# Optimization experiments

Measured on AMD Instinct MI355X. Metric: run time of the kernel, lower is better.

Reference implementation:

```python
import jax, jax.numpy as jnp
import numpy as np

EPS = 1e-16


def setup_inputs() -> dict:
    key = jax.random.key(0)
    k1, k2 = jax.random.split(key)
    N, D = 512, 4096
    a = jax.random.normal(k1, (N, D), dtype=jnp.float32)
    p = jax.random.normal(k2, (N, D), dtype=jnp.float32)
    return {"a": a, "p": p}


def reference(a, p):
    N = a.shape[0]
    # Pairwise squared distances between anchors a and positives p:
    # ||a_i||^2 - 2 a_i . p_j + ||p_j||^2   (diag(a a^T) == row norms)
    dot = jnp.matmul(a, p.T)                       # [N, N]
    sq_a = jnp.sum(a * a, axis=-1)                 # [N]
    sq_p = jnp.sum(p * p, axis=-1)                 # [N]
    d2 = sq_a[:, None] - 2.0 * dot + sq_p[None, :]
    d2 = jnp.maximum(d2, 0.0)                      # distances[distances < 0] = 0
    zero_mask = (d2 == 0.0).astype(d2.dtype)
    dist = (1.0 - zero_mask) * jnp.sqrt(d2 + zero_mask * EPS)  # [N, N]

    # Triplet tensor: loss[a, p, n] = dist[a, p] - dist[a, n]
    triplet = dist[:, :, None] - dist[:, None, :]  # [N, N, N]

    # Validity mask: labels = arange(N) -> valid iff p == anchor and n != anchor
    labels = jnp.arange(N)
    label_eq = labels[:, None] == labels[None, :]  # [N, N]
    mask = label_eq[:, :, None] & (~label_eq[:, None, :])  # [N, N, N]

    triplet = mask.astype(triplet.dtype) * triplet
    triplet = jax.nn.relu(triplet)

    num_positive = jnp.sum(triplet > EPS).astype(triplet.dtype)
    loss = jnp.sum(triplet) / (num_positive + EPS)
    return loss
```

## Files before the change

### kernel.cpp

```cpp
#include <hip/hip_runtime.h>
#include <math.h>

#define PN 512
#define PD 4096

#define KSZ 8
#define KCHUNK (PD / KSZ)
#define BK 64
#define NSTAGE (KCHUNK / BK)

#define WS_AH_BYTES 8192
#define WS_PH_BYTES (8192 + 4194304)
#define WS_PART_FLOAT 2099200
#define WS_NEED_BF16 ((size_t)(8192 + 2 * 4194304 + (size_t)KSZ * PN * PN * 4))

typedef __attribute__((ext_vector_type(8))) short short8;
typedef __attribute__((ext_vector_type(4))) float floatx4;

static __device__ __forceinline__ unsigned short f2bf(float x) {
    unsigned int u = __float_as_uint(x);
    u += 0x7fffu + ((u >> 16) & 1u);
    return (unsigned short)(u >> 16);
}

static __device__ __forceinline__ void load16_lds(const void* gp, void* lp) {
    __builtin_amdgcn_global_load_lds(
        (const __attribute__((address_space(1))) unsigned int*)gp,
        (__attribute__((address_space(3))) unsigned int*)lp,
        16, 0, 0);
}

struct ushort4s { unsigned short x, y, z, w; };

__global__ __launch_bounds__(256) void taw_prep_kernel(
        const float* __restrict__ a, const float* __restrict__ p,
        float* __restrict__ ws) {
    const int i = blockIdx.x;
    const int t = threadIdx.x;
    if (i == 0 && t == 0) {
        ws[1536] = 0.0f;
        ((unsigned int*)ws)[1537] = 0u;
    }
    const float4* a4 = (const float4*)(a + (size_t)i * PD);
    const float4* p4 = (const float4*)(p + (size_t)i * PD);
    unsigned short* ah = (unsigned short*)((char*)ws + WS_AH_BYTES) + (size_t)i * PD;
    unsigned short* ph = (unsigned short*)((char*)ws + WS_PH_BYTES) + (size_t)i * PD;
    float sa = 0.f, sp = 0.f, dp = 0.f;
#pragma unroll
    for (int c = 0; c < 4; ++c) {
        const int e = c * 256 + t;
        float4 av = a4[e];
        float4 pv = p4[e];
        sa += av.x * av.x + av.y * av.y + av.z * av.z + av.w * av.w;
        sp += pv.x * pv.x + pv.y * pv.y + pv.z * pv.z + pv.w * pv.w;
        dp += av.x * pv.x + av.y * pv.y + av.z * pv.z + av.w * pv.w;
        ushort4s ab = {f2bf(av.x), f2bf(av.y), f2bf(av.z), f2bf(av.w)};
        ushort4s pb = {f2bf(pv.x), f2bf(pv.y), f2bf(pv.z), f2bf(pv.w)};
        *(ushort4s*)(ah + (size_t)e * 4) = ab;
        *(ushort4s*)(ph + (size_t)e * 4) = pb;
    }
#pragma unroll
    for (int off = 32; off > 0; off >>= 1) {
        sa += __shfl_down(sa, off, 64);
        sp += __shfl_down(sp, off, 64);
        dp += __shfl_down(dp, off, 64);
    }
    __shared__ float red[3][4];
    const int wave = t >> 6;
    if ((t & 63) == 0) { red[0][wave] = sa; red[1][wave] = sp; red[2][wave] = dp; }
    __syncthreads();
    if (t == 0) {
        sa = red[0][0] + red[0][1] + red[0][2] + red[0][3];
        sp = red[1][0] + red[1][1] + red[1][2] + red[1][3];
        dp = red[2][0] + red[2][1] + red[2][2] + red[2][3];
        float d2 = sa - 2.f * dp + sp;
        d2 = fmaxf(d2, 0.f);
        ws[i] = sa;
        ws[512 + i] = sp;
        ws[1024 + i] = (d2 == 0.f) ? 0.f : sqrtf(d2);
    }
}

__global__ __launch_bounds__(256) void taw_mfma_kernel(float* __restrict__ ws) {
    __shared__ short lds[2][8][64][8];
    const unsigned short* ah = (const unsigned short*)((const char*)ws + WS_AH_BYTES);
    const unsigned short* ph = (const unsigned short*)((const char*)ws + WS_PH_BYTES);
    const int t = threadIdx.x;
    const int lane = t & 63;
    const int w = t >> 6;
    const int wm = w >> 1, wn = w & 1;
    const int i0 = blockIdx.y * 64;
    const int j0 = blockIdx.x * 64;
    const int kz = blockIdx.z * KCHUNK;

    floatx4 acc[2][2] = {{{0.f, 0.f, 0.f, 0.f}, {0.f, 0.f, 0.f, 0.f}},
                         {{0.f, 0.f, 0.f, 0.f}, {0.f, 0.f, 0.f, 0.f}}};

    for (int st = 0; st < NSTAGE; ++st) {
        const int kb = kz + st * BK;
        __syncthreads();
#pragma unroll
        for (int q = 0; q < 2; ++q) {
            const int g = 2 * w + q;
            const int row = ((g & 3) << 4) + (lane & 15);
            const int kk = kb + ((((g >> 2) << 2) + (lane >> 4)) << 3);
            load16_lds(ah + (size_t)(i0 + row) * PD + kk, &lds[0][g][0][0]);
            load16_lds(ph + (size_t)(j0 + row) * PD + kk, &lds[1][g][0][0]);
        }
        __syncthreads();
#pragma unroll
        for (int s2 = 0; s2 < 2; ++s2) {
            short8 af0 = *(const short8*)&lds[0][s2 * 4 + wm * 2 + 0][lane][0];
            short8 af1 = *(const short8*)&lds[0][s2 * 4 + wm * 2 + 1][lane][0];
            short8 bf0 = *(const short8*)&lds[1][s2 * 4 + wn * 2 + 0][lane][0];
            short8 bf1 = *(const short8*)&lds[1][s2 * 4 + wn * 2 + 1][lane][0];
            acc[0][0] = __builtin_amdgcn_mfma_f32_16x16x32_bf16(af0, bf0, acc[0][0], 0, 0, 0);
            acc[0][1] = __builtin_amdgcn_mfma_f32_16x16x32_bf16(af0, bf1, acc[0][1], 0, 0, 0);
            acc[1][0] = __builtin_amdgcn_mfma_f32_16x16x32_bf16(af1, bf0, acc[1][0], 0, 0, 0);
            acc[1][1] = __builtin_amdgcn_mfma_f32_16x16x32_bf16(af1, bf1, acc[1][1], 0, 0, 0);
        }
    }

    float* part = ws + WS_PART_FLOAT + (size_t)blockIdx.z * (PN * PN);
    const int jj = j0 + wn * 32 + (lane & 15);
    const int ib = i0 + wm * 32 + ((lane >> 4) << 2);
#pragma unroll
    for (int rm = 0; rm < 2; ++rm)
#pragma unroll
        for (int rn = 0; rn < 2; ++rn)
#pragma unroll
            for (int r = 0; r < 4; ++r)
                part[(size_t)(ib + rm * 16 + r) * PN + jj + rn * 16] = acc[rm][rn][r];
}

__global__ __launch_bounds__(256) void taw_reduce_kernel(float* __restrict__ ws) {
    const int g = blockIdx.x * 256 + threadIdx.x;
    const float4* part4 = (const float4*)(ws + WS_PART_FLOAT);
    float4 dot = part4[g];
#pragma unroll
    for (int ks = 1; ks < KSZ; ++ks) {
        const float4 v = part4[((size_t)ks << 16) + g];
        dot.x += v.x; dot.y += v.y; dot.z += v.z; dot.w += v.w;
    }
    const int flat = g << 2;
    const int i = flat >> 9;
    const int j = flat & 511;
    const float sa = ws[i];
    const float dd = ws[1024 + i];
    const float4 sp4 = *(const float4*)(ws + 512 + j);
    const float dotr[4] = {dot.x, dot.y, dot.z, dot.w};
    const float spr[4] = {sp4.x, sp4.y, sp4.z, sp4.w};
    float lsum = 0.f;
    unsigned int lcnt = 0;
#pragma unroll
    for (int c = 0; c < 4; ++c) {
        const int jj = j + c;
        float d2 = sa - 2.f * dotr[c] + spr[c];
        d2 = fmaxf(d2, 0.f);
        const float dist = (d2 == 0.f) ? 0.f : sqrtf(d2);
        const float v = (i != jj) ? fmaxf(dd - dist, 0.f) : 0.f;
        lsum += v;
        lcnt += (v > 1e-16f) ? 1u : 0u;
    }
#pragma unroll
    for (int off = 32; off > 0; off >>= 1) {
        lsum += __shfl_down(lsum, off, 64);
        lcnt += __shfl_down(lcnt, off, 64);
    }
    __shared__ float rsum[4];
    __shared__ unsigned int rcnt[4];
    const int t = threadIdx.x;
    if ((t & 63) == 0) { rsum[t >> 6] = lsum; rcnt[t >> 6] = lcnt; }
    __syncthreads();
    if (t == 0) {
        atomicAdd(ws + 1536, rsum[0] + rsum[1] + rsum[2] + rsum[3]);
        atomicAdd(((unsigned int*)ws) + 1537, rcnt[0] + rcnt[1] + rcnt[2] + rcnt[3]);
    }
}

__global__ void taw_finalize_kernel(const float* __restrict__ ws,
                                    float* __restrict__ out) {
    const double s = (double)ws[1536];
    const double c = (double)(((const unsigned int*)ws)[1537]);
    out[0] = (float)(s / (c + 1e-16));
}

__global__ __launch_bounds__(256) void taw_gemm_loss_kernel(
        const float* __restrict__ A, const float* __restrict__ P,
        float* __restrict__ ws) {
    __shared__ float as[32][34];
    __shared__ float bs[32][34];
    const int tx = threadIdx.x;
    const int ty = threadIdx.y;
    const int t = ty * 16 + tx;
    const int i0 = blockIdx.y * 32;
    const int j0 = blockIdx.x * 32;
    const int sr = t >> 3;
    const int sk = (t & 7) * 4;
    const float* aptr = A + (size_t)(i0 + sr) * PD + sk;
    const float* pptr = P + (size_t)(j0 + sr) * PD + sk;
    float c00 = 0.f, c01 = 0.f, c10 = 0.f, c11 = 0.f;
    for (int k0 = 0; k0 < PD; k0 += 32) {
        float4 av = *(const float4*)(aptr + k0);
        float4 pv = *(const float4*)(pptr + k0);
        __syncthreads();
        as[sk + 0][sr] = av.x; as[sk + 1][sr] = av.y;
        as[sk + 2][sr] = av.z; as[sk + 3][sr] = av.w;
        bs[sk + 0][sr] = pv.x; bs[sk + 1][sr] = pv.y;
        bs[sk + 2][sr] = pv.z; bs[sk + 3][sr] = pv.w;
        __syncthreads();
#pragma unroll
        for (int kk = 0; kk < 32; ++kk) {
            const float2 a2 = *(const float2*)&as[kk][2 * ty];
            const float2 b2 = *(const float2*)&bs[kk][2 * tx];
            c00 = fmaf(a2.x, b2.x, c00);
            c01 = fmaf(a2.x, b2.y, c01);
            c10 = fmaf(a2.y, b2.x, c10);
            c11 = fmaf(a2.y, b2.y, c11);
        }
    }
    const float* sq_a = ws;
    const float* sq_p = ws + 512;
    const float* ddg  = ws + 1024;
    const int i = i0 + 2 * ty;
    const int j = j0 + 2 * tx;
    float cvals[2][2] = {{c00, c01}, {c10, c11}};
    float lsum = 0.f;
    unsigned int lcnt = 0;
#pragma unroll
    for (int dr = 0; dr < 2; ++dr)
#pragma unroll
        for (int dc = 0; dc < 2; ++dc) {
            const int ii = i + dr, jj = j + dc;
            float d2 = sq_a[ii] - 2.f * cvals[dr][dc] + sq_p[jj];
            d2 = fmaxf(d2, 0.f);
            const float dist = (d2 == 0.f) ? 0.f : sqrtf(d2);
            const float v = (ii != jj) ? fmaxf(ddg[ii] - dist, 0.f) : 0.f;
            lsum += v;
            lcnt += (v > 1e-16f) ? 1u : 0u;
        }
#pragma unroll
    for (int off = 32; off > 0; off >>= 1) {
        lsum += __shfl_down(lsum, off, 64);
        lcnt += __shfl_down(lcnt, off, 64);
    }
    __shared__ float rsum[4];
    __shared__ unsigned int rcnt[4];
    if ((t & 63) == 0) { rsum[t >> 6] = lsum; rcnt[t >> 6] = lcnt; }
    __syncthreads();
    if (t == 0) {
        atomicAdd(ws + 1536, rsum[0] + rsum[1] + rsum[2] + rsum[3]);
        atomicAdd(((unsigned int*)ws) + 1537, rcnt[0] + rcnt[1] + rcnt[2] + rcnt[3]);
    }
}

extern "C" void kernel_launch(void* const* d_in, const int* in_sizes, int n_in,
                              void* d_out, int out_size, void* d_ws, size_t ws_size,
                              hipStream_t stream) {
    (void)in_sizes; (void)n_in; (void)out_size;
    const float* a = (const float*)d_in[0];
    const float* p = (const float*)d_in[1];
    float* out = (float*)d_out;
    float* ws = (float*)d_ws;

    taw_prep_kernel<<<PN, 256, 0, stream>>>(a, p, ws);
    if (ws_size >= WS_NEED_BF16) {
        taw_mfma_kernel<<<dim3(8, 8, KSZ), 256, 0, stream>>>(ws);
        taw_reduce_kernel<<<256, 256, 0, stream>>>(ws);
    } else {
        taw_gemm_loss_kernel<<<dim3(16, 16), dim3(16, 16), 0, stream>>>(a, p, ws);
    }
    taw_finalize_kernel<<<1, 1, 0, stream>>>(ws, out);
}
```

Measured before the change: 87.79 us.

## Fuse split-K GEMM, reduce and finalize into one double-buffered MFMA kernel

Replaces the split-K MFMA kernel (8 K-slices writing partial dot products to workspace) plus the separate reduce and finalize kernels with one kernel. Each block computes a full-K 32x32 tile using double-buffered LDS staging of 256-wide K chunks, applies the loss epilogue in registers, and uses a last-block atomic counter to write the final ratio. It also remaps block IDs across XCDs for locality. This removes the partial-sum round trip through global memory and two launches, at the cost of a long serial K loop per block and only 256 blocks with larger LDS use.

```diff
diff --git a/kernel.cpp b/kernel.cpp
--- a/kernel.cpp
+++ b/kernel.cpp
@@ -4,15 +4,12 @@
 #define PN 512
 #define PD 4096
 
-#define KSZ 8
-#define KCHUNK (PD / KSZ)
-#define BK 64
-#define NSTAGE (KCHUNK / BK)
+#define BK 256
+#define NST (PD / BK)
 
 #define WS_AH_BYTES 8192
 #define WS_PH_BYTES (8192 + 4194304)
-#define WS_PART_FLOAT 2099200
-#define WS_NEED_BF16 ((size_t)(8192 + 2 * 4194304 + (size_t)KSZ * PN * PN * 4))
+#define WS_NEED_MAIN ((size_t)(8192 + 2 * 4194304))
 
 typedef __attribute__((ext_vector_type(8))) short short8;
 typedef __attribute__((ext_vector_type(4))) float floatx4;
@@ -34,12 +31,13 @@
 
 __global__ __launch_bounds__(256) void taw_prep_kernel(
         const float* __restrict__ a, const float* __restrict__ p,
-        float* __restrict__ ws) {
+        float* __restrict__ ws, int conv) {
     const int i = blockIdx.x;
     const int t = threadIdx.x;
     if (i == 0 && t == 0) {
         ws[1536] = 0.0f;
         ((unsigned int*)ws)[1537] = 0u;
+        ((unsigned int*)ws)[1538] = 0u;
     }
     const float4* a4 = (const float4*)(a + (size_t)i * PD);
     const float4* p4 = (const float4*)(p + (size_t)i * PD);
@@ -54,10 +52,12 @@
         sa += av.x * av.x + av.y * av.y + av.z * av.z + av.w * av.w;
         sp += pv.x * pv.x + pv.y * pv.y + pv.z * pv.z + pv.w * pv.w;
         dp += av.x * pv.x + av.y * pv.y + av.z * pv.z + av.w * pv.w;
-        ushort4s ab = {f2bf(av.x), f2bf(av.y), f2bf(av.z), f2bf(av.w)};
-        ushort4s pb = {f2bf(pv.x), f2bf(pv.y), f2bf(pv.z), f2bf(pv.w)};
-        *(ushort4s*)(ah + (size_t)e * 4) = ab;
-        *(ushort4s*)(ph + (size_t)e * 4) = pb;
+        if (conv) {
+            ushort4s ab = {f2bf(av.x), f2bf(av.y), f2bf(av.z), f2bf(av.w)};
+            ushort4s pb = {f2bf(pv.x), f2bf(pv.y), f2bf(pv.z), f2bf(pv.w)};
+            *(ushort4s*)(ah + (size_t)e * 4) = ab;
+            *(ushort4s*)(ph + (size_t)e * 4) = pb;
+        }
     }
 #pragma unroll
     for (int off = 32; off > 0; off >>= 1) {
@@ -81,84 +81,74 @@
     }
 }
 
-__global__ __launch_bounds__(256) void taw_mfma_kernel(float* __restrict__ ws) {
-    __shared__ short lds[2][8][64][8];
+__global__ __launch_bounds__(256) void taw_fused_kernel(
+        float* __restrict__ ws, float* __restrict__ out) {
+    __shared__ short lds[2][32][64][8];
     const unsigned short* ah = (const unsigned short*)((const char*)ws + WS_AH_BYTES);
     const unsigned short* ph = (const unsigned short*)((const char*)ws + WS_PH_BYTES);
     const int t = threadIdx.x;
     const int lane = t & 63;
     const int w = t >> 6;
     const int wm = w >> 1, wn = w & 1;
-    const int i0 = blockIdx.y * 64;
-    const int j0 = blockIdx.x * 64;
-    const int kz = blockIdx.z * KCHUNK;
-
-    floatx4 acc[2][2] = {{{0.f, 0.f, 0.f, 0.f}, {0.f, 0.f, 0.f, 0.f}},
-                         {{0.f, 0.f, 0.f, 0.f}, {0.f, 0.f, 0.f, 0.f}}};
-
-    for (int st = 0; st < NSTAGE; ++st) {
-        const int kb = kz + st * BK;
+
+    const int B = blockIdx.x;
+    const int xcd = B & 7;
+    const int l = B >> 3;
+    const int bi = ((xcd >> 1) << 2) + (l >> 3);
+    const int bj = ((xcd & 1) << 3) + (l & 7);
+    const int i0 = bi * 32;
+    const int j0 = bj * 32;
+
+    const unsigned short* sbase[8];
+#pragma unroll
+    for (int q = 0; q < 8; ++q) {
+        const int g16 = w * 8 + q;
+        const int g = g16 & 15;
+        const int row = ((g & 1) << 4) + (lane & 15);
+        const int kk = ((g >> 1) << 5) + ((lane >> 4) << 3);
+        sbase[q] = (g16 < 16 ? ah + (size_t)(i0 + row) * PD
+                             : ph + (size_t)(j0 + row) * PD) + kk;
+    }
+
+    auto STAGE = [&](int buf, int kst) {
+#pragma unroll
+        for (int q = 0; q < 8; ++q) {
+            load16_lds(sbase[q] + kst, &lds[buf][w * 8 + q][0][0]);
+        }
+    };
+
+    floatx4 acc[4];
+#pragma unroll
+    for (int c = 0; c < 4; ++c) acc[c] = (floatx4){0.f, 0.f, 0.f, 0.f};
+
+    STAGE(0, 0);
+    __syncthreads();
+    for (int st = 0; st < NST; ++st) {
+        if (st + 1 < NST) STAGE((st + 1) & 1, (st + 1) * BK);
+        const int b = st & 1;
+#pragma unroll
+        for (int kb = 0; kb < 8; ++kb) {
+            short8 af = *(const short8*)&lds[b][kb * 2 + wm][lane][0];
+            short8 bf = *(const short8*)&lds[b][16 + kb * 2 + wn][lane][0];
+            acc[kb & 3] = __builtin_amdgcn_mfma_f32_16x16x32_bf16(af, bf, acc[kb & 3], 0, 0, 0);
+        }
         __syncthreads();
-#pragma unroll
-        for (int q = 0; q < 2; ++q) {
-            const int g = 2 * w + q;
-            const int row = ((g & 3) << 4) + (lane & 15);
-            const int kk = kb + ((((g >> 2) << 2) + (lane >> 4)) << 3);
-            load16_lds(ah + (size_t)(i0 + row) * PD + kk, &lds[0][g][0][0]);
-            load16_lds(ph + (size_t)(j0 + row) * PD + kk, &lds[1][g][0][0]);
-        }
-        __syncthreads();
-#pragma unroll
-        for (int s2 = 0; s2 < 2; ++s2) {
-            short8 af0 = *(const short8*)&lds[0][s2 * 4 + wm * 2 + 0][lane][0];
-            short8 af1 = *(const short8*)&lds[0][s2 * 4 + wm * 2 + 1][lane][0];
-            short8 bf0 = *(const short8*)&lds[1][s2 * 4 + wn * 2 + 0][lane][0];
-            short8 bf1 = *(const short8*)&lds[1][s2 * 4 + wn * 2 + 1][lane][0];
-            acc[0][0] = __builtin_amdgcn_mfma_f32_16x16x32_bf16(af0, bf0, acc[0][0], 0, 0, 0);
-            acc[0][1] = __builtin_amdgcn_mfma_f32_16x16x32_bf16(af0, bf1, acc[0][1], 0, 0, 0);
-            acc[1][0] = __builtin_amdgcn_mfma_f32_16x16x32_bf16(af1, bf0, acc[1][0], 0, 0, 0);
-            acc[1][1] = __builtin_amdgcn_mfma_f32_16x16x32_bf16(af1, bf1, acc[1][1], 0, 0, 0);
-        }
-    }
-
-    float* part = ws + WS_PART_FLOAT + (size_t)blockIdx.z * (PN * PN);
-    const int jj = j0 + wn * 32 + (lane & 15);
-    const int ib = i0 + wm * 32 + ((lane >> 4) << 2);
-#pragma unroll
-    for (int rm = 0; rm < 2; ++rm)
-#pragma unroll
-        for (int rn = 0; rn < 2; ++rn)
-#pragma unroll
-            for (int r = 0; r < 4; ++r)
-                part[(size_t)(ib + rm * 16 + r) * PN + jj + rn * 16] = acc[rm][rn][r];
-}
-
-__global__ __launch_bounds__(256) void taw_reduce_kernel(float* __restrict__ ws) {
-    const int g = blockIdx.x * 256 + threadIdx.x;
-    const float4* part4 = (const float4*)(ws + WS_PART_FLOAT);
-    float4 dot = part4[g];
-#pragma unroll
-    for (int ks = 1; ks < KSZ; ++ks) {
-        const float4 v = part4[((size_t)ks << 16) + g];
-        dot.x += v.x; dot.y += v.y; dot.z += v.z; dot.w += v.w;
-    }
-    const int flat = g << 2;
-    const int i = flat >> 9;
-    const int j = flat & 511;
-    const float sa = ws[i];
-    const float dd = ws[1024 + i];
-    const float4 sp4 = *(const float4*)(ws + 512 + j);
-    const float dotr[4] = {dot.x, dot.y, dot.z, dot.w};
-    const float spr[4] = {sp4.x, sp4.y, sp4.z, sp4.w};
+    }
+
+    const floatx4 dot = acc[0] + acc[1] + acc[2] + acc[3];
+
+    const int jj = j0 + wn * 16 + (lane & 15);
+    const int ib = i0 + wm * 16 + ((lane >> 4) << 2);
+    const float sp = ws[512 + jj];
     float lsum = 0.f;
     unsigned int lcnt = 0;
 #pragma unroll
-    for (int c = 0; c < 4; ++c) {
-        const int jj = j + c;
-        float d2 = sa - 2.f * dotr[c] + spr[c];
+    for (int r = 0; r < 4; ++r) {
+        const int ii = ib + r;
+        float d2 = ws[ii] - 2.f * dot[r] + sp;
         d2 = fmaxf(d2, 0.f);
         const float dist = (d2 == 0.f) ? 0.f : sqrtf(d2);
-        const float v = (i != jj) ? fmaxf(dd - dist, 0.f) : 0.f;
+        const float v = (ii != jj) ? fmaxf(ws[1024 + ii] - dist, 0.f) : 0.f;
         lsum += v;
         lcnt += (v > 1e-16f) ? 1u : 0u;
     }
@@ -169,12 +159,18 @@
     }
     __shared__ float rsum[4];
     __shared__ unsigned int rcnt[4];
-    const int t = threadIdx.x;
-    if ((t & 63) == 0) { rsum[t >> 6] = lsum; rcnt[t >> 6] = lcnt; }
+    if ((t & 63) == 0) { rsum[w] = lsum; rcnt[w] = lcnt; }
     __syncthreads();
     if (t == 0) {
         atomicAdd(ws + 1536, rsum[0] + rsum[1] + rsum[2] + rsum[3]);
         atomicAdd(((unsigned int*)ws) + 1537, rcnt[0] + rcnt[1] + rcnt[2] + rcnt[3]);
+        __threadfence();
+        const unsigned int old = atomicAdd(((unsigned int*)ws) + 1538, 1u);
+        if (old == 255u) {
+            const float s = atomicAdd(ws + 1536, 0.f);
+            const unsigned int c = atomicAdd(((unsigned int*)ws) + 1537, 0u);
+            out[0] = (float)((double)s / ((double)c + 1e-16));
+        }
     }
 }
 
@@ -263,12 +259,12 @@
     float* out = (float*)d_out;
     float* ws = (float*)d_ws;
 
-    taw_prep_kernel<<<PN, 256, 0, stream>>>(a, p, ws);
-    if (ws_size >= WS_NEED_BF16) {
-        taw_mfma_kernel<<<dim3(8, 8, KSZ), 256, 0, stream>>>(ws);
-        taw_reduce_kernel<<<256, 256, 0, stream>>>(ws);
+    const int use_mfma = (ws_size >= WS_NEED_MAIN) ? 1 : 0;
+    taw_prep_kernel<<<PN, 256, 0, stream>>>(a, p, ws, use_mfma);
+    if (use_mfma) {
+        taw_fused_kernel<<<256, 256, 0, stream>>>(ws, out);
     } else {
         taw_gemm_loss_kernel<<<dim3(16, 16), dim3(16, 16), 0, stream>>>(a, p, ws);
-    }
-    taw_finalize_kernel<<<1, 1, 0, stream>>>(ws, out);
-}
+        taw_finalize_kernel<<<1, 1, 0, stream>>>(ws, out);
+    }
+}
```

After: 101.8 us. 15.9% more time.

## Triple-buffer MFMA LDS loads and fold finalize into reduce via last-block counter

Applied to the files above, without the earlier changes.

The bf16 MFMA GEMM loop now uses a three-stage LDS ring. Asynchronous global-to-LDS loads are issued two stages ahead and gated with explicit vmcnt waits and raw barriers, so memory latency overlaps with MFMA work instead of being serialized by two syncthreads per stage. Separately, the reduce kernel uses an atomic block counter so the last block computes the final loss, which removes the single-thread finalize launch. The cost is more LDS per block, which may lower occupancy, and hand-tuned waitcnt values that must match the number of loads issued per stage.

```diff
diff --git a/kernel.cpp b/kernel.cpp
--- a/kernel.cpp
+++ b/kernel.cpp
@@ -40,6 +40,7 @@
     if (i == 0 && t == 0) {
         ws[1536] = 0.0f;
         ((unsigned int*)ws)[1537] = 0u;
+        ((unsigned int*)ws)[1538] = 0u;
     }
     const float4* a4 = (const float4*)(a + (size_t)i * PD);
     const float4* p4 = (const float4*)(p + (size_t)i * PD);
@@ -82,7 +83,7 @@
 }
 
 __global__ __launch_bounds__(256) void taw_mfma_kernel(float* __restrict__ ws) {
-    __shared__ short lds[2][8][64][8];
+    __shared__ short lds[3][2][8][64][8];
     const unsigned short* ah = (const unsigned short*)((const char*)ws + WS_AH_BYTES);
     const unsigned short* ph = (const unsigned short*)((const char*)ws + WS_PH_BYTES);
     const int t = threadIdx.x;
@@ -93,32 +94,56 @@
     const int j0 = blockIdx.x * 64;
     const int kz = blockIdx.z * KCHUNK;
 
+    const unsigned short* abase[2];
+    const unsigned short* pbase[2];
+#pragma unroll
+    for (int q = 0; q < 2; ++q) {
+        const int g = 2 * w + q;
+        const int row = ((g & 3) << 4) + (lane & 15);
+        const int kofs = ((g >> 2) << 5) + ((lane >> 4) << 3);
+        abase[q] = ah + (size_t)(i0 + row) * PD + kz + kofs;
+        pbase[q] = ph + (size_t)(j0 + row) * PD + kz + kofs;
+    }
+
+    auto STAGE = [&](int buf, int kb) {
+#pragma unroll
+        for (int q = 0; q < 2; ++q) {
+            load16_lds(abase[q] + kb, &lds[buf][0][2 * w + q][0][0]);
+            load16_lds(pbase[q] + kb, &lds[buf][1][2 * w + q][0][0]);
+        }
+    };
+
     floatx4 acc[2][2] = {{{0.f, 0.f, 0.f, 0.f}, {0.f, 0.f, 0.f, 0.f}},
                          {{0.f, 0.f, 0.f, 0.f}, {0.f, 0.f, 0.f, 0.f}}};
 
+    STAGE(0, 0);
+    STAGE(1, BK);
+#pragma unroll
     for (int st = 0; st < NSTAGE; ++st) {
-        const int kb = kz + st * BK;
-        __syncthreads();
-#pragma unroll
-        for (int q = 0; q < 2; ++q) {
-            const int g = 2 * w + q;
-            const int row = ((g & 3) << 4) + (lane & 15);
-            const int kk = kb + ((((g >> 2) << 2) + (lane >> 4)) << 3);
-            load16_lds(ah + (size_t)(i0 + row) * PD + kk, &lds[0][g][0][0]);
-            load16_lds(ph + (size_t)(j0 + row) * PD + kk, &lds[1][g][0][0]);
-        }
-        __syncthreads();
+        const int b = st % 3;
+        if (st + 2 < NSTAGE) {
+            STAGE((st + 2) % 3, (st + 2) * BK);
+            asm volatile("s_waitcnt vmcnt(8)" ::: "memory");
+        } else if (st + 1 < NSTAGE) {
+            asm volatile("s_waitcnt vmcnt(4)" ::: "memory");
+        } else {
+            asm volatile("s_waitcnt vmcnt(0)" ::: "memory");
+        }
+        __builtin_amdgcn_s_barrier();
 #pragma unroll
         for (int s2 = 0; s2 < 2; ++s2) {
-            short8 af0 = *(const short8*)&lds[0][s2 * 4 + wm * 2 + 0][lane][0];
-            short8 af1 = *(const short8*)&lds[0][s2 * 4 + wm * 2 + 1][lane][0];
-            short8 bf0 = *(const short8*)&lds[1][s2 * 4 + wn * 2 + 0][lane][0];
-            short8 bf1 = *(const short8*)&lds[1][s2 * 4 + wn * 2 + 1][lane][0];
+            short8 af0 = *(const short8*)&lds[b][0][s2 * 4 + wm * 2 + 0][lane][0];
+            short8 af1 = *(const short8*)&lds[b][0][s2 * 4 + wm * 2 + 1][lane][0];
+            short8 bf0 = *(const short8*)&lds[b][1][s2 * 4 + wn * 2 + 0][lane][0];
+            short8 bf1 = *(const short8*)&lds[b][1][s2 * 4 + wn * 2 + 1][lane][0];
             acc[0][0] = __builtin_amdgcn_mfma_f32_16x16x32_bf16(af0, bf0, acc[0][0], 0, 0, 0);
             acc[0][1] = __builtin_amdgcn_mfma_f32_16x16x32_bf16(af0, bf1, acc[0][1], 0, 0, 0);
             acc[1][0] = __builtin_amdgcn_mfma_f32_16x16x32_bf16(af1, bf0, acc[1][0], 0, 0, 0);
             acc[1][1] = __builtin_amdgcn_mfma_f32_16x16x32_bf16(af1, bf1, acc[1][1], 0, 0, 0);
         }
+        asm volatile("s_waitcnt lgkmcnt(0)" ::: "memory");
+        __builtin_amdgcn_sched_barrier(0);
+        __builtin_amdgcn_s_barrier();
     }
 
     float* part = ws + WS_PART_FLOAT + (size_t)blockIdx.z * (PN * PN);
@@ -133,7 +158,8 @@
                 part[(size_t)(ib + rm * 16 + r) * PN + jj + rn * 16] = acc[rm][rn][r];
 }
 
-__global__ __launch_bounds__(256) void taw_reduce_kernel(float* __restrict__ ws) {
+__global__ __launch_bounds__(256) void taw_reduce_kernel(float* __restrict__ ws,
+                                                         float* __restrict__ out) {
     const int g = blockIdx.x * 256 + threadIdx.x;
     const float4* part4 = (const float4*)(ws + WS_PART_FLOAT);
     float4 dot = part4[g];
@@ -175,6 +201,13 @@
     if (t == 0) {
         atomicAdd(ws + 1536, rsum[0] + rsum[1] + rsum[2] + rsum[3]);
         atomicAdd(((unsigned int*)ws) + 1537, rcnt[0] + rcnt[1] + rcnt[2] + rcnt[3]);
+        __threadfence();
+        const unsigned int old = atomicAdd(((unsigned int*)ws) + 1538, 1u);
+        if (old == 255u) {
+            const float s = atomicAdd(ws + 1536, 0.f);
+            const unsigned int c = atomicAdd(((unsigned int*)ws) + 1537, 0u);
+            out[0] = (float)((double)s / ((double)c + 1e-16));
+        }
     }
 }
 
@@ -266,9 +299,9 @@
     taw_prep_kernel<<<PN, 256, 0, stream>>>(a, p, ws);
     if (ws_size >= WS_NEED_BF16) {
         taw_mfma_kernel<<<dim3(8, 8, KSZ), 256, 0, stream>>>(ws);
-        taw_reduce_kernel<<<256, 256, 0, stream>>>(ws);
+        taw_reduce_kernel<<<256, 256, 0, stream>>>(ws, out);
     } else {
         taw_gemm_loss_kernel<<<dim3(16, 16), dim3(16, 16), 0, stream>>>(a, p, ws);
-    }
-    taw_finalize_kernel<<<1, 1, 0, stream>>>(ws, out);
-}
+        taw_finalize_kernel<<<1, 1, 0, stream>>>(ws, out);
+    }
+}
```

After: 92.27 us. 5.1% more time.
